# Performance work log

Measured on AMD Instinct MI355X. Metric: run time of the kernel, lower is better.

## Reference

```python
import jax, jax.numpy as jnp
import numpy as np

N, E = 50000, 800000
IN_DIM, HID_DIM, OUT_DIM = 512, 256, 128


def setup_inputs() -> dict:
    key = jax.random.key(0)
    ks = jax.random.split(key, 10)
    x = jax.random.normal(ks[0], (N, IN_DIM), dtype=jnp.float32)
    edge_index = jax.random.randint(ks[1], (2, E), 0, N, dtype=jnp.int64)
    edge_weight = jax.random.uniform(ks[2], (E,), dtype=jnp.float32)
    # GCNConv weights (PyG stores weight as [in, out]; out = x @ W + b)
    def glorot(k, fan_in, fan_out):
        lim = np.sqrt(6.0 / (fan_in + fan_out)).astype(np.float32)
        return jax.random.uniform(k, (fan_in, fan_out), minval=-lim, maxval=lim, dtype=jnp.float32)
    W1 = glorot(ks[3], IN_DIM, HID_DIM)
    b1 = jnp.zeros((HID_DIM,), dtype=jnp.float32)
    W2 = glorot(ks[4], HID_DIM, OUT_DIM)
    b2 = jnp.zeros((OUT_DIM,), dtype=jnp.float32)
    Wp = glorot(ks[5], OUT_DIM, OUT_DIM)
    bp = jnp.zeros((OUT_DIM,), dtype=jnp.float32)
    return {"x": x, "edge_index": edge_index, "edge_weight": edge_weight,
            "W1": W1, "b1": b1, "W2": W2, "b2": b2, "Wp": Wp, "bp": bp}


def _gcn_norm(edge_index, edge_weight, n_nodes):
    # add self loops with weight 1.0 (PyG gcn_norm, fill_value=1.0)
    loops = jnp.arange(n_nodes, dtype=edge_index.dtype)
    row = jnp.concatenate([edge_index[0], loops])
    col = jnp.concatenate([edge_index[1], loops])
    w = jnp.concatenate([edge_weight, jnp.ones((n_nodes,), edge_weight.dtype)])
    deg = jax.ops.segment_sum(w, col, num_segments=n_nodes)  # [N]
    dinv = jnp.where(deg > 0, jax.lax.rsqrt(deg), 0.0)
    norm = dinv[row] * w * dinv[col]  # [E+N]
    return row, col, norm


def _gcn_conv(h, row, col, norm, W, b, n_nodes):
    h = h @ W                              # [N, out]
    msgs = h[row] * norm[:, None]          # gather + scale  [E+N, out]
    out = jax.ops.segment_sum(msgs, col, num_segments=n_nodes)  # scatter-add
    return out + b


def reference(x, edge_index, edge_weight, W1, b1, W2, b2, Wp, bp):
    n_nodes = x.shape[0]
    # eval mode: F.dropout(edge_weight, training=False) is identity
    row, col, norm = _gcn_norm(edge_index, edge_weight, n_nodes)
    h = jax.nn.relu(_gcn_conv(x, row, col, norm, W1, b1, n_nodes))
    # eval mode: F.dropout identity
    h = _gcn_conv(h, row, col, norm, W2, b2, n_nodes)
    return h @ Wp + bp
```

## Files before the change

kernel.cpp:

```cpp
#include <hip/hip_runtime.h>

#define IN_DIM 512
#define HID_DIM 256
#define OUT_DIM 128
#define BCAP 64

typedef unsigned short u16;
typedef __attribute__((ext_vector_type(8))) short bf16x8;
typedef __attribute__((ext_vector_type(4))) float f32x4;

__device__ inline u16 f2bf(float f) {
    unsigned u = __float_as_uint(f);
    return (u16)((u + 0x7FFFu + ((u >> 16) & 1u)) >> 16);
}
__device__ inline float bf2f(u16 u) {
    return __uint_as_float(((unsigned)u) << 16);
}

__device__ inline void gld_lds16(const void* g, void* l) {
    __builtin_amdgcn_global_load_lds((const __attribute__((address_space(1))) unsigned*)g,
                                     (__attribute__((address_space(3))) unsigned*)l, 16, 0, 0);
}


__global__ void bucket_fill_kernel(const int* __restrict__ row, const int* __restrict__ col,
                                   const float* __restrict__ w,
                                   int* __restrict__ cnt, int2* __restrict__ bucket, int E) {
    int e = blockIdx.x * blockDim.x + threadIdx.x;
    if (e >= E) return;
    int c = col[e];
    int slot = atomicAdd(&cnt[c], 1);
    if (slot < BCAP) {
        int2 v;
        v.x = row[e];
        v.y = __float_as_int(w[e]);
        bucket[(size_t)c * BCAP + slot] = v;
    }
}

__global__ void deg_dinv_kernel(const int2* __restrict__ bucket, const int* __restrict__ cnt,
                                float* __restrict__ dinv, int n) {
    int i = blockIdx.x * blockDim.x + threadIdx.x;
    if (i >= n) return;
    int c = min(cnt[i], BCAP);
    const int2* b = bucket + (size_t)i * BCAP;
    float s = 1.0f;
    for (int p = 0; p < c; ++p) s += __int_as_float(b[p].y);
    dinv[i] = (s > 0.0f) ? rsqrtf(s) : 0.0f;
}


__global__ __launch_bounds__(256)
void weight_prep_kernel(const float* __restrict__ W1, u16* __restrict__ W1T,
                        const float* __restrict__ W2, const float* __restrict__ Wp,
                        const float* __restrict__ b2, const float* __restrict__ bp,
                        u16* __restrict__ W2pT, float* __restrict__ bias2,
                        int nW1, int nW2p) {
    const int b = blockIdx.x;
    const int tid = threadIdx.x;
    if (b < nW1) {
        int idx = b * 256 + tid;
        if (idx >= IN_DIM * HID_DIM) return;
        int nrow = idx / IN_DIM, k = idx - nrow * IN_DIM;
        W1T[idx] = f2bf(W1[(size_t)k * HID_DIM + nrow]);
        return;
    }
    if (b < nW1 + nW2p) {
        int idx = (b - nW1) * 256 + tid;
        if (idx >= OUT_DIM * HID_DIM) return;
        int n = idx / HID_DIM, k = idx - n * HID_DIM;
        float s = 0.0f;
        for (int m = 0; m < OUT_DIM; ++m)
            s = fmaf(W2[(size_t)k * OUT_DIM + m], Wp[(size_t)m * OUT_DIM + n], s);
        W2pT[idx] = f2bf(s);
        return;
    }
    if (tid < OUT_DIM) {
        float s = bp[tid];
        for (int m = 0; m < OUT_DIM; ++m)
            s = fmaf(b2[m], Wp[(size_t)m * OUT_DIM + tid], s);
        bias2[tid] = s;
    }
}


#define TM 128
#define TN 128
#define TK 32

template <typename AT, typename OutT>
__global__ __launch_bounds__(256)
void mfma_gemm_kernel(const AT* __restrict__ A, const u16* __restrict__ BT,
                      const float* __restrict__ bias, OutT* __restrict__ C,
                      int Mreal, int Mpad, int Nc, int K) {
    __shared__ u16 As[TM * TK];
    __shared__ u16 Bs[TN * TK];
    const int tid = threadIdx.x;
    const int w = tid >> 6, l = tid & 63;
    const int wr = w >> 1, wc = w & 1;
    const long tile_m = (long)blockIdx.x * TM;
    const int tile_n = blockIdx.y * TN;

    const int r0 = w * 32 + (l >> 2);
    const int r1 = r0 + 16;
    const int c0 = l & 3;
    const long gb0 = (long)(tile_n + r0) * K + (long)((c0 ^ (r0 & 3)) * 8);
    const long gb1 = (long)(tile_n + r1) * K + (long)((c0 ^ (r1 & 3)) * 8);
    u16* ldsB0 = &Bs[(w * 2 + 0) * 512];
    u16* ldsB1 = &Bs[(w * 2 + 1) * 512];

    const long ga0 = (tile_m + r0) * (long)K + (long)((c0 ^ (r0 & 3)) * 8);
    const long ga1 = (tile_m + r1) * (long)K + (long)((c0 ^ (r1 & 3)) * 8);
    u16* ldsA0 = &As[(w * 2 + 0) * 512];
    u16* ldsA1 = &As[(w * 2 + 1) * 512];

    const int ci0 = tid, ci1 = tid + 256;
    const int arow0 = ci0 >> 2, ach0 = ci0 & 3;
    const int arow1 = ci1 >> 2, ach1 = ci1 & 3;
    const int ag0 = (ach0 ^ (arow0 & 3)) * 8;
    const int ag1 = (ach1 ^ (arow1 & 3)) * 8;

    f32x4 acc[4][4] = {};
    const int lr = l & 15;
    const int kl = l >> 4;

    for (int k0 = 0; k0 < K; k0 += TK) {
        if (k0) __syncthreads();
        if constexpr (sizeof(AT) == 4) {
            float4 f0a = {0,0,0,0}, f0b = {0,0,0,0}, f1a = {0,0,0,0}, f1b = {0,0,0,0};
            if (tile_m + arow0 < Mreal) {
                const float* s0 = (const float*)A + (tile_m + arow0) * (long)K + k0 + ag0;
                f0a = *(const float4*)s0; f0b = *(const float4*)(s0 + 4);
            }
            if (tile_m + arow1 < Mreal) {
                const float* s1 = (const float*)A + (tile_m + arow1) * (long)K + k0 + ag1;
                f1a = *(const float4*)s1; f1b = *(const float4*)(s1 + 4);
            }
            int4 w0, w1;
            w0.x = f2bf(f0a.x) | ((unsigned)f2bf(f0a.y) << 16);
            w0.y = f2bf(f0a.z) | ((unsigned)f2bf(f0a.w) << 16);
            w0.z = f2bf(f0b.x) | ((unsigned)f2bf(f0b.y) << 16);
            w0.w = f2bf(f0b.z) | ((unsigned)f2bf(f0b.w) << 16);
            w1.x = f2bf(f1a.x) | ((unsigned)f2bf(f1a.y) << 16);
            w1.y = f2bf(f1a.z) | ((unsigned)f2bf(f1a.w) << 16);
            w1.z = f2bf(f1b.x) | ((unsigned)f2bf(f1b.y) << 16);
            w1.w = f2bf(f1b.z) | ((unsigned)f2bf(f1b.w) << 16);
            *(int4*)((char*)As + arow0 * 64 + ach0 * 16) = w0;
            *(int4*)((char*)As + arow1 * 64 + ach1 * 16) = w1;
        } else {
            gld_lds16((const u16*)A + ga0 + k0, ldsA0);
            gld_lds16((const u16*)A + ga1 + k0, ldsA1);
        }
        gld_lds16(BT + gb0 + k0, ldsB0);
        gld_lds16(BT + gb1 + k0, ldsB1);
        __syncthreads();

        bf16x8 af[4], bfv[4];
#pragma unroll
        for (int mi = 0; mi < 4; ++mi) {
            int rowi = wr * 64 + mi * 16 + lr;
            int byte = rowi * 64 + ((kl ^ (rowi & 3)) * 16);
            af[mi] = *(const bf16x8*)((const char*)As + byte);
        }
#pragma unroll
        for (int ni = 0; ni < 4; ++ni) {
            int rowi = wc * 64 + ni * 16 + lr;
            int byte = rowi * 64 + ((kl ^ (rowi & 3)) * 16);
            bfv[ni] = *(const bf16x8*)((const char*)Bs + byte);
        }
#pragma unroll
        for (int mi = 0; mi < 4; ++mi)
#pragma unroll
            for (int ni = 0; ni < 4; ++ni)
                acc[mi][ni] = __builtin_amdgcn_mfma_f32_16x16x32_bf16(af[mi], bfv[ni], acc[mi][ni], 0, 0, 0);
    }

    float bv[4];
#pragma unroll
    for (int ni = 0; ni < 4; ++ni)
        bv[ni] = bias ? bias[tile_n + wc * 64 + ni * 16 + lr] : 0.0f;
#pragma unroll
    for (int mi = 0; mi < 4; ++mi) {
#pragma unroll
        for (int reg = 0; reg < 4; ++reg) {
            long rowg = tile_m + wr * 64 + mi * 16 + kl * 4 + reg;
            if (rowg < Mpad) {
#pragma unroll
                for (int ni = 0; ni < 4; ++ni) {
                    int colc = tile_n + wc * 64 + ni * 16 + lr;
                    float v = acc[mi][ni][reg] + bv[ni];
                    if constexpr (sizeof(OutT) == 2) C[rowg * Nc + colc] = f2bf(v);
                    else                             C[rowg * Nc + colc] = v;
                }
            }
        }
    }
}


template <int DIM, bool RELU, typename OutT>
__global__ __launch_bounds__(256)
void aggregate_kernel(const u16* __restrict__ t,
                      const int2* __restrict__ bucket,
                      const int* __restrict__ cnt,
                      const float* __restrict__ dinv,
                      const float* __restrict__ bias,
                      OutT* __restrict__ outp, int n) {
    constexpr int V = DIM / 64;
    const int wv = threadIdx.x >> 6;
    const int l = threadIdx.x & 63;
    const int node = blockIdx.x * 4 + wv;
    if (node >= n) return;
    const float dv = dinv[node];
    const float dv2 = dv * dv;
    float acc[V];
    if constexpr (V == 4) {
        ushort4 q = *(const ushort4*)(t + (size_t)node * DIM + l * 4);
        acc[0] = dv2 * bf2f(q.x); acc[1] = dv2 * bf2f(q.y);
        acc[2] = dv2 * bf2f(q.z); acc[3] = dv2 * bf2f(q.w);
    } else {
        ushort2 q = *(const ushort2*)(t + (size_t)node * DIM + l * 2);
        acc[0] = dv2 * bf2f(q.x); acc[1] = dv2 * bf2f(q.y);
    }
    const int e = min(cnt[node], BCAP);
    const int2* b = bucket + (size_t)node * BCAP;
    int p = 0;
    for (; p + 8 <= e; p += 8) {
        int2 ed[8];
        float wt[8];
#pragma unroll
        for (int j = 0; j < 8; ++j) ed[j] = b[p + j];
#pragma unroll
        for (int j = 0; j < 8; ++j) wt[j] = dv * __int_as_float(ed[j].y) * dinv[ed[j].x];
        if constexpr (V == 4) {
            ushort4 q[8];
#pragma unroll
            for (int j = 0; j < 8; ++j) q[j] = *(const ushort4*)(t + (size_t)ed[j].x * DIM + l * 4);
#pragma unroll
            for (int j = 0; j < 8; ++j) {
                acc[0] = fmaf(wt[j], bf2f(q[j].x), acc[0]);
                acc[1] = fmaf(wt[j], bf2f(q[j].y), acc[1]);
                acc[2] = fmaf(wt[j], bf2f(q[j].z), acc[2]);
                acc[3] = fmaf(wt[j], bf2f(q[j].w), acc[3]);
            }
        } else {
            ushort2 q[8];
#pragma unroll
            for (int j = 0; j < 8; ++j) q[j] = *(const ushort2*)(t + (size_t)ed[j].x * DIM + l * 2);
#pragma unroll
            for (int j = 0; j < 8; ++j) {
                acc[0] = fmaf(wt[j], bf2f(q[j].x), acc[0]);
                acc[1] = fmaf(wt[j], bf2f(q[j].y), acc[1]);
            }
        }
    }
    for (; p + 4 <= e; p += 4) {
        int2 ed[4];
        float wt[4];
#pragma unroll
        for (int j = 0; j < 4; ++j) ed[j] = b[p + j];
#pragma unroll
        for (int j = 0; j < 4; ++j) wt[j] = dv * __int_as_float(ed[j].y) * dinv[ed[j].x];
        if constexpr (V == 4) {
            ushort4 q[4];
#pragma unroll
            for (int j = 0; j < 4; ++j) q[j] = *(const ushort4*)(t + (size_t)ed[j].x * DIM + l * 4);
#pragma unroll
            for (int j = 0; j < 4; ++j) {
                acc[0] = fmaf(wt[j], bf2f(q[j].x), acc[0]);
                acc[1] = fmaf(wt[j], bf2f(q[j].y), acc[1]);
                acc[2] = fmaf(wt[j], bf2f(q[j].z), acc[2]);
                acc[3] = fmaf(wt[j], bf2f(q[j].w), acc[3]);
            }
        } else {
            ushort2 q[4];
#pragma unroll
            for (int j = 0; j < 4; ++j) q[j] = *(const ushort2*)(t + (size_t)ed[j].x * DIM + l * 2);
#pragma unroll
            for (int j = 0; j < 4; ++j) {
                acc[0] = fmaf(wt[j], bf2f(q[j].x), acc[0]);
                acc[1] = fmaf(wt[j], bf2f(q[j].y), acc[1]);
            }
        }
    }
    for (; p < e; ++p) {
        int2 e0 = b[p];
        float wgt = dv * __int_as_float(e0.y) * dinv[e0.x];
        if constexpr (V == 4) {
            ushort4 q = *(const ushort4*)(t + (size_t)e0.x * DIM + l * 4);
            acc[0] = fmaf(wgt, bf2f(q.x), acc[0]); acc[1] = fmaf(wgt, bf2f(q.y), acc[1]);
            acc[2] = fmaf(wgt, bf2f(q.z), acc[2]); acc[3] = fmaf(wgt, bf2f(q.w), acc[3]);
        } else {
            ushort2 q = *(const ushort2*)(t + (size_t)e0.x * DIM + l * 2);
            acc[0] = fmaf(wgt, bf2f(q.x), acc[0]); acc[1] = fmaf(wgt, bf2f(q.y), acc[1]);
        }
    }
#pragma unroll
    for (int j = 0; j < V; ++j) {
        float v = acc[j] + bias[l * V + j];
        if (RELU) v = fmaxf(v, 0.0f);
        acc[j] = v;
    }
    if constexpr (sizeof(OutT) == 2) {
        if constexpr (V == 4) {
            ushort4 st;
            st.x = f2bf(acc[0]); st.y = f2bf(acc[1]); st.z = f2bf(acc[2]); st.w = f2bf(acc[3]);
            *(ushort4*)((u16*)outp + (size_t)node * DIM + l * 4) = st;
        } else {
            ushort2 st;
            st.x = f2bf(acc[0]); st.y = f2bf(acc[1]);
            *(ushort2*)((u16*)outp + (size_t)node * DIM + l * 2) = st;
        }
    } else {
        if constexpr (V == 4) {
            float4 st = {acc[0], acc[1], acc[2], acc[3]};
            *(float4*)((float*)outp + (size_t)node * DIM + l * 4) = st;
        } else {
            float2 st = {acc[0], acc[1]};
            *(float2*)((float*)outp + (size_t)node * DIM + l * 2) = st;
        }
    }
}


extern "C" void kernel_launch(void* const* d_in, const int* in_sizes, int n_in,
                              void* d_out, int out_size, void* d_ws, size_t ws_size,
                              hipStream_t stream) {
    const float* x  = (const float*)d_in[0];
    const int*   ei = (const int*)d_in[1];
    const float* ew = (const float*)d_in[2];
    const float* W1 = (const float*)d_in[3];
    const float* b1 = (const float*)d_in[4];
    const float* W2 = (const float*)d_in[5];
    const float* b2 = (const float*)d_in[6];
    const float* Wp = (const float*)d_in[7];
    const float* bp = (const float*)d_in[8];
    float* out = (float*)d_out;

    const int E = in_sizes[2];
    const int N = in_sizes[0] / IN_DIM;
    const int Mpad = ((N + TM - 1) / TM) * TM;
    const int* row = ei;
    const int* col = ei + E;

    size_t off = 0;
    auto carve = [&](size_t bytes) -> void* {
        void* p = (char*)d_ws + off;
        off += (bytes + 255) & ~(size_t)255;
        return p;
    };
    float* dinv   = (float*)carve((size_t)N * 4);
    int*   cnt    = (int*)carve((size_t)N * 4);
    int2*  bucket = (int2*)carve((size_t)N * BCAP * 8);
    u16*   W1T    = (u16*)carve((size_t)HID_DIM * IN_DIM * 2);
    u16*   W2pT   = (u16*)carve((size_t)OUT_DIM * HID_DIM * 2);
    float* bias2  = (float*)carve((size_t)OUT_DIM * 4);
    u16*   bufA   = (u16*)carve((size_t)Mpad * HID_DIM * 2);
    u16*   bufB   = (u16*)carve((size_t)Mpad * HID_DIM * 2);

    u16* t1 = bufB;
    u16* a1 = bufA;
    u16* t3 = bufB;

    const int TB = 256;
    const int gN = (N + TB - 1) / TB;
    const int gE = (E + TB - 1) / TB;

    const int nW1  = (IN_DIM * HID_DIM + TB - 1) / TB;
    const int nW2p = (OUT_DIM * HID_DIM + TB - 1) / TB;

    hipMemsetAsync(cnt, 0, (size_t)N * 4, stream);
    bucket_fill_kernel<<<gE, TB, 0, stream>>>(row, col, ew, cnt, bucket, E);
    weight_prep_kernel<<<nW1 + nW2p + 1, TB, 0, stream>>>(W1, W1T, W2, Wp, b2, bp, W2pT, bias2, nW1, nW2p);
    deg_dinv_kernel<<<gN, TB, 0, stream>>>(bucket, cnt, dinv, N);

    const int gm = Mpad / TM;
    const int gagg = (N + 3) / 4;

    mfma_gemm_kernel<float, u16><<<dim3(gm, HID_DIM / TN), 256, 0, stream>>>(x, W1T, nullptr, t1, N, Mpad, HID_DIM, IN_DIM);
    aggregate_kernel<HID_DIM, true, u16><<<gagg, 256, 0, stream>>>(t1, bucket, cnt, dinv, b1, a1, N);
    mfma_gemm_kernel<u16, u16><<<dim3(gm, OUT_DIM / TN), 256, 0, stream>>>(a1, W2pT, nullptr, t3, N, Mpad, OUT_DIM, HID_DIM);
    aggregate_kernel<OUT_DIM, false, float><<<gagg, 256, 0, stream>>>(t3, bucket, cnt, dinv, bias2, out, N);
}
```

Baseline: 370.3 us.

## Double-buffer GEMM LDS tiles and change the XOR swizzle pattern

The MFMA GEMM now uses two LDS buffers for the A and B tiles. The next K-tile's global loads (register prefetch for fp32 A, direct-to-LDS for bf16 A and B) are issued before the current tile's MFMAs, so memory latency overlaps with compute and one barrier per iteration is removed. The LDS swizzle also changes from row&3 to (row>>1)&3 to reduce bank conflicts on the 16-byte fragment reads. In exchange, LDS use doubles and the prefetched fp32 values hold extra registers, which may lower occupancy.

```diff
diff --git a/kernel.cpp b/kernel.cpp
--- a/kernel.cpp
+++ b/kernel.cpp
@@ -93,8 +93,8 @@
 void mfma_gemm_kernel(const AT* __restrict__ A, const u16* __restrict__ BT,
                       const float* __restrict__ bias, OutT* __restrict__ C,
                       int Mreal, int Mpad, int Nc, int K) {
-    __shared__ u16 As[TM * TK];
-    __shared__ u16 Bs[TN * TK];
+    __shared__ u16 As[2][TM * TK];
+    __shared__ u16 Bs[2][TN * TK];
     const int tid = threadIdx.x;
     const int w = tid >> 6, l = tid & 63;
     const int wr = w >> 1, wc = w & 1;
@@ -104,75 +104,93 @@
     const int r0 = w * 32 + (l >> 2);
     const int r1 = r0 + 16;
     const int c0 = l & 3;
-    const long gb0 = (long)(tile_n + r0) * K + (long)((c0 ^ (r0 & 3)) * 8);
-    const long gb1 = (long)(tile_n + r1) * K + (long)((c0 ^ (r1 & 3)) * 8);
-    u16* ldsB0 = &Bs[(w * 2 + 0) * 512];
-    u16* ldsB1 = &Bs[(w * 2 + 1) * 512];
-
-    const long ga0 = (tile_m + r0) * (long)K + (long)((c0 ^ (r0 & 3)) * 8);
-    const long ga1 = (tile_m + r1) * (long)K + (long)((c0 ^ (r1 & 3)) * 8);
-    u16* ldsA0 = &As[(w * 2 + 0) * 512];
-    u16* ldsA1 = &As[(w * 2 + 1) * 512];
-
-    const int ci0 = tid, ci1 = tid + 256;
-    const int arow0 = ci0 >> 2, ach0 = ci0 & 3;
-    const int arow1 = ci1 >> 2, ach1 = ci1 & 3;
-    const int ag0 = (ach0 ^ (arow0 & 3)) * 8;
-    const int ag1 = (ach1 ^ (arow1 & 3)) * 8;
+    const long gb0 = (long)(tile_n + r0) * K + (long)((c0 ^ ((r0 >> 1) & 3)) * 8);
+    const long gb1 = (long)(tile_n + r1) * K + (long)((c0 ^ ((r1 >> 1) & 3)) * 8);
+    const long ga0 = (tile_m + r0) * (long)K + (long)((c0 ^ ((r0 >> 1) & 3)) * 8);
+    const long ga1 = (tile_m + r1) * (long)K + (long)((c0 ^ ((r1 >> 1) & 3)) * 8);
+
+    const int arow0 = tid >> 2, ach0 = tid & 3;
+    const int arow1 = arow0 + 64;
+    const int ag0 = (ach0 ^ ((arow0 >> 1) & 3)) * 8;
+    const int ag1 = (ach0 ^ ((arow1 >> 1) & 3)) * 8;
+
+    float4 pfa = {0,0,0,0}, pfb = {0,0,0,0}, pfc = {0,0,0,0}, pfd = {0,0,0,0};
+    auto loadA = [&](int k0) {
+        pfa = pfb = pfc = pfd = float4{0, 0, 0, 0};
+        if (tile_m + arow0 < Mreal) {
+            const float* s0 = (const float*)A + (tile_m + arow0) * (long)K + k0 + ag0;
+            pfa = *(const float4*)s0; pfb = *(const float4*)(s0 + 4);
+        }
+        if (tile_m + arow1 < Mreal) {
+            const float* s1 = (const float*)A + (tile_m + arow1) * (long)K + k0 + ag1;
+            pfc = *(const float4*)s1; pfd = *(const float4*)(s1 + 4);
+        }
+    };
+    auto writeA = [&](int buf) {
+        int4 w0, w1;
+        w0.x = f2bf(pfa.x) | ((unsigned)f2bf(pfa.y) << 16);
+        w0.y = f2bf(pfa.z) | ((unsigned)f2bf(pfa.w) << 16);
+        w0.z = f2bf(pfb.x) | ((unsigned)f2bf(pfb.y) << 16);
+        w0.w = f2bf(pfb.z) | ((unsigned)f2bf(pfb.w) << 16);
+        w1.x = f2bf(pfc.x) | ((unsigned)f2bf(pfc.y) << 16);
+        w1.y = f2bf(pfc.z) | ((unsigned)f2bf(pfc.w) << 16);
+        w1.z = f2bf(pfd.x) | ((unsigned)f2bf(pfd.y) << 16);
+        w1.w = f2bf(pfd.z) | ((unsigned)f2bf(pfd.w) << 16);
+        *(int4*)((char*)&As[buf][0] + arow0 * 64 + ach0 * 16) = w0;
+        *(int4*)((char*)&As[buf][0] + arow1 * 64 + ach0 * 16) = w1;
+    };
+    auto stageA16 = [&](int k0, int buf) {
+        gld_lds16((const u16*)A + ga0 + k0, &As[buf][(w * 2 + 0) * 512]);
+        gld_lds16((const u16*)A + ga1 + k0, &As[buf][(w * 2 + 1) * 512]);
+    };
+    auto stageB = [&](int k0, int buf) {
+        gld_lds16(BT + gb0 + k0, &Bs[buf][(w * 2 + 0) * 512]);
+        gld_lds16(BT + gb1 + k0, &Bs[buf][(w * 2 + 1) * 512]);
+    };
 
     f32x4 acc[4][4] = {};
     const int lr = l & 15;
     const int kl = l >> 4;
 
-    for (int k0 = 0; k0 < K; k0 += TK) {
-        if (k0) __syncthreads();
-        if constexpr (sizeof(AT) == 4) {
-            float4 f0a = {0,0,0,0}, f0b = {0,0,0,0}, f1a = {0,0,0,0}, f1b = {0,0,0,0};
-            if (tile_m + arow0 < Mreal) {
-                const float* s0 = (const float*)A + (tile_m + arow0) * (long)K + k0 + ag0;
-                f0a = *(const float4*)s0; f0b = *(const float4*)(s0 + 4);
-            }
-            if (tile_m + arow1 < Mreal) {
-                const float* s1 = (const float*)A + (tile_m + arow1) * (long)K + k0 + ag1;
-                f1a = *(const float4*)s1; f1b = *(const float4*)(s1 + 4);
-            }
-            int4 w0, w1;
-            w0.x = f2bf(f0a.x) | ((unsigned)f2bf(f0a.y) << 16);
-            w0.y = f2bf(f0a.z) | ((unsigned)f2bf(f0a.w) << 16);
-            w0.z = f2bf(f0b.x) | ((unsigned)f2bf(f0b.y) << 16);
-            w0.w = f2bf(f0b.z) | ((unsigned)f2bf(f0b.w) << 16);
-            w1.x = f2bf(f1a.x) | ((unsigned)f2bf(f1a.y) << 16);
-            w1.y = f2bf(f1a.z) | ((unsigned)f2bf(f1a.w) << 16);
-            w1.z = f2bf(f1b.x) | ((unsigned)f2bf(f1b.y) << 16);
-            w1.w = f2bf(f1b.z) | ((unsigned)f2bf(f1b.w) << 16);
-            *(int4*)((char*)As + arow0 * 64 + ach0 * 16) = w0;
-            *(int4*)((char*)As + arow1 * 64 + ach1 * 16) = w1;
-        } else {
-            gld_lds16((const u16*)A + ga0 + k0, ldsA0);
-            gld_lds16((const u16*)A + ga1 + k0, ldsA1);
-        }
-        gld_lds16(BT + gb0 + k0, ldsB0);
-        gld_lds16(BT + gb1 + k0, ldsB1);
-        __syncthreads();
+    if constexpr (sizeof(AT) == 4) { loadA(0); writeA(0); }
+    else stageA16(0, 0);
+    stageB(0, 0);
+    __syncthreads();
+
+    const int NT = K / TK;
+    for (int t = 0; t < NT; ++t) {
+        const int cur = t & 1, nxt = cur ^ 1;
+        const bool more = (t + 1 < NT);
+        const int k1 = (t + 1) * TK;
+        if (more) {
+            if constexpr (sizeof(AT) == 4) loadA(k1);
+            else stageA16(k1, nxt);
+            stageB(k1, nxt);
+        }
 
         bf16x8 af[4], bfv[4];
 #pragma unroll
         for (int mi = 0; mi < 4; ++mi) {
             int rowi = wr * 64 + mi * 16 + lr;
-            int byte = rowi * 64 + ((kl ^ (rowi & 3)) * 16);
-            af[mi] = *(const bf16x8*)((const char*)As + byte);
+            int byte = rowi * 64 + ((kl ^ ((rowi >> 1) & 3)) * 16);
+            af[mi] = *(const bf16x8*)((const char*)&As[cur][0] + byte);
         }
 #pragma unroll
         for (int ni = 0; ni < 4; ++ni) {
             int rowi = wc * 64 + ni * 16 + lr;
-            int byte = rowi * 64 + ((kl ^ (rowi & 3)) * 16);
-            bfv[ni] = *(const bf16x8*)((const char*)Bs + byte);
+            int byte = rowi * 64 + ((kl ^ ((rowi >> 1) & 3)) * 16);
+            bfv[ni] = *(const bf16x8*)((const char*)&Bs[cur][0] + byte);
         }
 #pragma unroll
         for (int mi = 0; mi < 4; ++mi)
 #pragma unroll
             for (int ni = 0; ni < 4; ++ni)
                 acc[mi][ni] = __builtin_amdgcn_mfma_f32_16x16x32_bf16(af[mi], bfv[ni], acc[mi][ni], 0, 0, 0);
+
+        if constexpr (sizeof(AT) == 4) {
+            if (more) writeA(nxt);
+        }
+        __syncthreads();
     }
 
     float bv[4];
```

Result: slower. 381.2 us (+3.0%).
